# Performance work log

Measured on AMD Instinct MI355X. Metric: run time of the kernel, lower is better.

Reference implementation:

```python
import jax, jax.numpy as jnp
import numpy as np

N_NODES = 64
HIDDEN = 16
SCALE = HIDDEN ** -0.5
NEG_INF = -1e9


def setup_inputs() -> dict:
    key = jax.random.key(0)
    ks = jax.random.split(key, 5)
    x = jax.random.normal(ks[0], (256, 1, N_NODES, 4096), dtype=jnp.float32)
    wq = jax.random.normal(ks[1], (HIDDEN,), dtype=jnp.float32)
    bq = jax.random.normal(ks[2], (HIDDEN,), dtype=jnp.float32)
    wk = jax.random.normal(ks[3], (HIDDEN,), dtype=jnp.float32)
    bk = jax.random.normal(ks[4], (HIDDEN,), dtype=jnp.float32)
    return {"x": x, "wq": wq, "bq": bq, "wk": wk, "bk": bk}


def reference(x, wq, bq, wk, bk):
    xs = x[:, 0]                                   # (B, 64, T)
    # torch.var defaults to unbiased (ddof=1)
    e = jnp.var(xs, axis=-1, ddof=1)               # (B, 64)
    # Conv1d(1, H, k=1) == per-channel affine: (B, H, 64)
    Q = wq[None, :, None] * e[:, None, :] + bq[None, :, None]
    K = wk[None, :, None] * e[:, None, :] + bk[None, :, None]
    attn = jnp.einsum('bhi,bhj->bij', Q, K) * SCALE  # (B, 64, 64)
    eye = jnp.eye(N_NODES, dtype=bool)
    attn = jnp.where(eye[None], NEG_INF, attn)
    attn_weights = jax.nn.softmax(attn, axis=-1)
    out = jnp.einsum('bij,bjt->bit', attn_weights, xs)  # (B, 64, T)
    return out[:, None] + x, attn_weights
```

## Files before the change

### kernel.cpp

```cpp
#include <hip/hip_runtime.h>

#define NB 256
#define NN 64
#define NT 4096

__global__ __launch_bounds__(256) void var_kernel(const float* __restrict__ x,
                                                  float* __restrict__ e) {
    int row  = blockIdx.x * 4 + (threadIdx.x >> 6);
    int lane = threadIdx.x & 63;
    const float4* xr = (const float4*)(x + (size_t)row * NT);
    float s = 0.f, ss = 0.f;
#pragma unroll
    for (int k = 0; k < 16; ++k) {
        float4 v = xr[lane + k * 64];
        s  += (v.x + v.y) + (v.z + v.w);
        ss += (v.x * v.x + v.y * v.y) + (v.z * v.z + v.w * v.w);
    }
#pragma unroll
    for (int off = 32; off > 0; off >>= 1) {
        s  += __shfl_down(s, off);
        ss += __shfl_down(ss, off);
    }
    if (lane == 0) {
        float mean = s * (1.0f / NT);
        e[row] = (ss - (float)NT * mean * mean) * (1.0f / (NT - 1));
    }
}

__global__ __launch_bounds__(64) void attn_kernel(const float* __restrict__ e,
                                                  const float* __restrict__ wq,
                                                  const float* __restrict__ bq,
                                                  const float* __restrict__ wk,
                                                  const float* __restrict__ bk,
                                                  float* __restrict__ attn_out,
                                                  float* __restrict__ wpT) {
    int b = blockIdx.x;
    int i = threadIdx.x;
    float A = 0.f, Bq = 0.f, Bk = 0.f, C = 0.f;
#pragma unroll
    for (int h = 0; h < 16; ++h) {
        A  += wq[h] * wk[h];
        Bq += wq[h] * bk[h];
        Bk += bq[h] * wk[h];
        C  += bq[h] * bk[h];
    }
    __shared__ float es[NN];
    es[i] = e[b * NN + i];
    __syncthreads();
    float ei = es[i];
    float l[NN];
    float m = -3.0e38f;
#pragma unroll
    for (int j = 0; j < NN; ++j) {
        float v = 0.25f * (A * ei * es[j] + Bq * ei + Bk * es[j] + C);
        if (j == i) v = -1.0e9f;
        l[j] = v;
        m = fmaxf(m, v);
    }
    float sum = 0.f;
#pragma unroll
    for (int j = 0; j < NN; ++j) {
        float ev = expf(l[j] - m);
        l[j] = ev;
        sum += ev;
    }
    float inv = 1.0f / sum;
    float* dst = attn_out + (size_t)b * (NN * NN) + i * NN;
    float* wt  = wpT      + (size_t)b * (NN * NN);
#pragma unroll
    for (int j = 0; j < NN; ++j) {
        float w = l[j] * inv;
        dst[j] = w;
        wt[j * NN + i] = (j == i) ? 1.0f : w;
    }
}

__global__ __launch_bounds__(256) void out_kernel(const float* __restrict__ x,
                                                  const float* __restrict__ WpT,
                                                  float* __restrict__ out) {
    int blk = blockIdx.x;
    int b = blk >> 4;
    int t = (blk & 15) * 256 + threadIdx.x;
    const float* xb = x + (size_t)b * (NN * NT) + t;
    const float* Wb = WpT + (size_t)b * (NN * NN);

    float acc[NN];
#pragma unroll
    for (int i = 0; i < NN; ++i) acc[i] = 0.f;

#pragma unroll 2
    for (int j = 0; j < NN; ++j) {
        float xv = xb[(size_t)j * NT];
        const float* Wr = Wb + j * NN;
#pragma unroll
        for (int i = 0; i < NN; ++i) acc[i] = fmaf(Wr[i], xv, acc[i]);
    }

    float* ob = out + (size_t)b * (NN * NT) + t;
#pragma unroll
    for (int i = 0; i < NN; ++i) ob[(size_t)i * NT] = acc[i];
}

extern "C" void kernel_launch(void* const* d_in, const int* in_sizes, int n_in,
                              void* d_out, int out_size, void* d_ws, size_t ws_size,
                              hipStream_t stream) {
    const float* x  = (const float*)d_in[0];
    const float* wq = (const float*)d_in[1];
    const float* bq = (const float*)d_in[2];
    const float* wk = (const float*)d_in[3];
    const float* bk = (const float*)d_in[4];
    float* out  = (float*)d_out;
    float* attn = out + (size_t)NB * NN * NT;
    float* e    = (float*)d_ws;
    float* wpT  = (float*)d_ws + NB * NN;

    var_kernel<<<NB * NN / 4, 256, 0, stream>>>(x, e);
    attn_kernel<<<NB, 64, 0, stream>>>(e, wq, bq, wk, bk, attn, wpT);
    out_kernel<<<NB * 16, 256, 0, stream>>>(x, wpT, out);
}
```

Before: 575.7 us.

## Stage weights in LDS and split output rows across waves with float4 columns

The output kernel now copies the per-batch 64x64 weight matrix into shared memory, gives each of 8 waves 8 output rows, and has each lane handle 4 consecutive time columns using float4 loads and stores. This removes the 64-accumulator-per-thread register pressure and the scalar global weight reads. The cost is that each wave re-reads the x stripe, so x is loaded 8 times per block (mostly from cache). The attention kernel also transposes its weights through shared memory so that global stores to attn_out are coalesced.

Measured after the change: 553.0 us. 1.04x faster.

```diff
diff --git a/kernel.cpp b/kernel.cpp
--- a/kernel.cpp
+++ b/kernel.cpp
@@ -45,6 +45,7 @@
         C  += bq[h] * bk[h];
     }
     __shared__ float es[NN];
+    __shared__ float tr[NN][NN + 1];
     es[i] = e[b * NN + i];
     __syncthreads();
     float ei = es[i];
@@ -65,40 +66,65 @@
         sum += ev;
     }
     float inv = 1.0f / sum;
-    float* dst = attn_out + (size_t)b * (NN * NN) + i * NN;
-    float* wt  = wpT      + (size_t)b * (NN * NN);
+    float* wt = wpT + (size_t)b * (NN * NN);
 #pragma unroll
     for (int j = 0; j < NN; ++j) {
         float w = l[j] * inv;
-        dst[j] = w;
+        tr[i][j] = w;
         wt[j * NN + i] = (j == i) ? 1.0f : w;
     }
+    __syncthreads();
+    float* dst = attn_out + (size_t)b * (NN * NN);
+#pragma unroll
+    for (int r = 0; r < NN; ++r)
+        dst[r * NN + i] = tr[r][i];
 }
 
-__global__ __launch_bounds__(256) void out_kernel(const float* __restrict__ x,
-                                                  const float* __restrict__ WpT,
-                                                  float* __restrict__ out) {
+__global__ __launch_bounds__(512, 2) void out_kernel(const float* __restrict__ x,
+                                                     const float* __restrict__ WpT,
+                                                     float* __restrict__ out) {
+    __shared__ float sW[NN * NN];
     int blk = blockIdx.x;
     int b = blk >> 4;
-    int t = (blk & 15) * 256 + threadIdx.x;
+    int stripe = blk & 15;
+    int tid = threadIdx.x;
+    int wave = tid >> 6;
+    int lane = tid & 63;
+
+    {
+        const float4* src = (const float4*)(WpT + (size_t)b * (NN * NN));
+        float4* dst = (float4*)sW;
+        dst[tid]       = src[tid];
+        dst[tid + 512] = src[tid + 512];
+    }
+    __syncthreads();
+
+    int t = stripe * 256 + lane * 4;
     const float* xb = x + (size_t)b * (NN * NT) + t;
-    const float* Wb = WpT + (size_t)b * (NN * NN);
 
-    float acc[NN];
+    float4 acc[8];
 #pragma unroll
-    for (int i = 0; i < NN; ++i) acc[i] = 0.f;
+    for (int r = 0; r < 8; ++r) acc[r] = make_float4(0.f, 0.f, 0.f, 0.f);
 
-#pragma unroll 2
+    const float* sWr = sW + wave * 8;
+#pragma unroll 8
     for (int j = 0; j < NN; ++j) {
-        float xv = xb[(size_t)j * NT];
-        const float* Wr = Wb + j * NN;
+        float4 xv = *(const float4*)(xb + (size_t)j * NT);
+        const float* w = sWr + j * NN;
 #pragma unroll
-        for (int i = 0; i < NN; ++i) acc[i] = fmaf(Wr[i], xv, acc[i]);
+        for (int r = 0; r < 8; ++r) {
+            float wr = w[r];
+            acc[r].x = fmaf(wr, xv.x, acc[r].x);
+            acc[r].y = fmaf(wr, xv.y, acc[r].y);
+            acc[r].z = fmaf(wr, xv.z, acc[r].z);
+            acc[r].w = fmaf(wr, xv.w, acc[r].w);
+        }
     }
 
-    float* ob = out + (size_t)b * (NN * NT) + t;
+    float* ob = out + (size_t)b * (NN * NT) + (size_t)(wave * 8) * NT + t;
 #pragma unroll
-    for (int i = 0; i < NN; ++i) ob[(size_t)i * NT] = acc[i];
+    for (int r = 0; r < 8; ++r)
+        *(float4*)(ob + (size_t)r * NT) = acc[r];
 }
 
 extern "C" void kernel_launch(void* const* d_in, const int* in_sizes, int n_in,
@@ -116,5 +142,5 @@
 
     var_kernel<<<NB * NN / 4, 256, 0, stream>>>(x, e);
     attn_kernel<<<NB, 64, 0, stream>>>(e, wq, bq, wk, bk, attn, wpT);
-    out_kernel<<<NB * 16, 256, 0, stream>>>(x, wpT, out);
+    out_kernel<<<NB * 16, 512, 0, stream>>>(x, wpT, out);
 }
```
